# Kernel tuning notes

Measured on AMD Instinct MI355X. Metric: run time of the kernel, lower is better.

Reference implementation:

```python
import jax, jax.numpy as jnp
import numpy as np

NUM_LAYERS = 4
HID = 512
EMB = 512
VOCAB = 50000
SOU_LEN = 256
TAR_LEN = 50
BATCH = 8
VEXT = VOCAB + SOU_LEN


def _gru_layer(x, h0, wih, whh, bih, bhh):
    # x: [B,T,in], h0: [B,H]; PyTorch GRU gate order: r, z, n
    def step(h, xt):
        gi = xt @ wih.T + bih
        gh = h @ whh.T + bhh
        ir, iz, inn = jnp.split(gi, 3, axis=-1)
        hr, hz, hn = jnp.split(gh, 3, axis=-1)
        r = jax.nn.sigmoid(ir + hr)
        z = jax.nn.sigmoid(iz + hz)
        n = jnp.tanh(inn + r * hn)
        h_new = (1.0 - z) * n + z * h
        return h_new, h_new
    _, ys = jax.lax.scan(step, h0, jnp.swapaxes(x, 0, 1))
    return jnp.swapaxes(ys, 0, 1)


def _forward(sou, tar, hidden, encoder_outputs, extended_length,
             emb, gru_wih, gru_whh, gru_bih, gru_bhh,
             fc_enc_w, fc_enc_b, fc_dec_w, fc_dec_b, v_w,
             fc_out1_w, fc_out1_b, fc_out2_w, fc_out2_b,
             g1_w, g1_b, g2_w, g2_b, g3_w, g3_b):
    emb = emb.at[0].set(0.0)  # padding_idx=0 (also zeroes its grad)
    tar_emb = emb[tar]  # [B,T,E]
    # pack_padded_sequence: only first `length` steps processed, rest padded with 0
    lengths = jnp.maximum(jnp.sum(tar > 0, axis=-1), 1)
    x = tar_emb
    for l in range(gru_wih.shape[0]):
        x = _gru_layer(x, hidden[l], gru_wih[l], gru_whh[l], gru_bih[l], gru_bhh[l])
    t_idx = jnp.arange(x.shape[1])
    dec_out = jnp.where((t_idx[None, :] < lengths[:, None])[:, :, None], x, 0.0)  # [B,T,H]
    # additive (Bahdanau) attention
    e1 = encoder_outputs @ fc_enc_w.T + fc_enc_b          # [B,S,H]
    e2 = dec_out @ fc_dec_w.T + fc_dec_b                  # [B,T,H]
    energy = jnp.tanh(e1[:, None, :, :] + e2[:, :, None, :])  # [B,T,S,H]
    scores = jnp.einsum('btsh,h->bts', energy, v_w)
    scores = jnp.where((sou == 0)[:, None, :], -jnp.inf, scores)
    atten = jax.nn.softmax(scores, axis=-1)               # [B,T,S]
    weighted = jnp.einsum('bts,bsh->bth', atten, encoder_outputs)
    all_out = jnp.concatenate([weighted, dec_out], axis=-1)  # [B,T,2H]
    mid = all_out @ fc_out2_w.T + fc_out2_b
    logits = mid @ fc_out1_w.T + fc_out1_b                # [B,T,VEXT]
    # extended-vocab mask (vectorized version of the per-batch python loop)
    col = jnp.arange(logits.shape[-1])
    valid = col[None, None, :] < (VOCAB + extended_length)[:, None, None]
    logits = jnp.where(valid, logits, -1e9)
    output_gen = jax.nn.softmax(logits, axis=-1)
    # copy mechanism: scatter-add attention into extended vocab (replaces sparse one-hot bmm)
    def _scatter(att_b, sou_b):
        return jnp.zeros((att_b.shape[0], VEXT), att_b.dtype).at[:, sou_b].add(att_b)
    output_copy = jax.vmap(_scatter)(atten, sou)          # [B,T,VEXT]
    gate = jax.nn.sigmoid(
        jnp.einsum('bth,h->bt', weighted, g1_w) + g1_b[0]
        + jnp.einsum('bth,h->bt', dec_out, g2_w) + g2_b[0]
        + jnp.einsum('bte,e->bt', tar_emb, g3_w) + g3_b[0])[:, :, None]
    output = (1.0 - gate) * output_gen + gate * output_copy
    return output, atten


def setup_inputs() -> dict:
    key = jax.random.key(0)
    ks = jax.random.split(key, 24)
    s = 0.02
    return {
        'sou': jax.random.randint(ks[0], (BATCH, SOU_LEN), 0, VEXT),
        'tar': jax.random.randint(ks[1], (BATCH, TAR_LEN), 0, VEXT),
        'hidden': jax.random.normal(ks[2], (NUM_LAYERS, BATCH, HID), jnp.float32),
        'encoder_outputs': jax.random.normal(ks[3], (BATCH, SOU_LEN, HID), jnp.float32),
        'extended_length': jax.random.randint(ks[4], (BATCH,), 0, SOU_LEN),
        'emb': jax.random.normal(ks[5], (VEXT, EMB), jnp.float32) * s,
        'gru_wih': jax.random.normal(ks[6], (NUM_LAYERS, 3 * HID, EMB), jnp.float32) * s,
        'gru_whh': jax.random.normal(ks[7], (NUM_LAYERS, 3 * HID, HID), jnp.float32) * s,
        'gru_bih': jax.random.normal(ks[8], (NUM_LAYERS, 3 * HID), jnp.float32) * s,
        'gru_bhh': jax.random.normal(ks[9], (NUM_LAYERS, 3 * HID), jnp.float32) * s,
        'fc_enc_w': jax.random.normal(ks[10], (HID, HID), jnp.float32) * s,
        'fc_enc_b': jax.random.normal(ks[11], (HID,), jnp.float32) * s,
        'fc_dec_w': jax.random.normal(ks[12], (HID, HID), jnp.float32) * s,
        'fc_dec_b': jax.random.normal(ks[13], (HID,), jnp.float32) * s,
        'v_w': jax.random.normal(ks[14], (HID,), jnp.float32) * s,
        'fc_out1_w': jax.random.normal(ks[15], (VEXT, HID), jnp.float32) * s,
        'fc_out1_b': jax.random.normal(ks[16], (VEXT,), jnp.float32) * s,
        'fc_out2_w': jax.random.normal(ks[17], (HID, 2 * HID), jnp.float32) * s,
        'fc_out2_b': jax.random.normal(ks[18], (HID,), jnp.float32) * s,
        'g1_w': jax.random.normal(ks[19], (HID,), jnp.float32) * s,
        'g1_b': jnp.zeros((1,), jnp.float32),
        'g2_w': jax.random.normal(ks[20], (HID,), jnp.float32) * s,
        'g2_b': jnp.zeros((1,), jnp.float32),
        'g3_w': jax.random.normal(ks[21], (EMB,), jnp.float32) * s,
        'g3_b': jnp.zeros((1,), jnp.float32),
    }


def reference(sou, tar, hidden, encoder_outputs, extended_length,
              emb, gru_wih, gru_whh, gru_bih, gru_bhh,
              fc_enc_w, fc_enc_b, fc_dec_w, fc_dec_b, v_w,
              fc_out1_w, fc_out1_b, fc_out2_w, fc_out2_b,
              g1_w, g1_b, g2_w, g2_b, g3_w, g3_b):
    return _forward(sou, tar, hidden, encoder_outputs, extended_length,
                    emb, gru_wih, gru_whh, gru_bih, gru_bhh,
                    fc_enc_w, fc_enc_b, fc_dec_w, fc_dec_b, v_w,
                    fc_out1_w, fc_out1_b, fc_out2_w, fc_out2_b,
                    g1_w, g1_b, g2_w, g2_b, g3_w, g3_b)
```

## Files before the change

kernel.cpp:

```cpp
#include <hip/hip_runtime.h>

typedef unsigned short u16;
typedef unsigned int u32;

using bf16x8 = __attribute__((ext_vector_type(8))) short;
using f32x4  = __attribute__((ext_vector_type(4))) float;

#define VOCAB 50000
#define VEXT  50256
#define OUT_AT_OFF 20102400L

__device__ __forceinline__ u16 f2b(float f) {
  u32 x = __float_as_uint(f);
  u32 r = (x + 0x7fffu + ((x >> 16) & 1u)) >> 16;
  return (u16)r;
}

__global__ void k_conv(const float* __restrict__ src, u16* __restrict__ dst,
                       long realN, long totalN) {
  long i = (long)blockIdx.x * 256 + threadIdx.x;
  if (i >= totalN) return;
  float v = (i < realN) ? src[i] : 0.f;
  dst[i] = f2b(v);
}

__global__ void k_h0b(const float* __restrict__ hidden, u16* __restrict__ h0B) {
  int i = blockIdx.x * 256 + threadIdx.x;
  int l = i >> 13, rem = i & 8191, rr = rem >> 9, k = rem & 511;
  float v = (rr < 8) ? hidden[((long)l * 8 + rr) * 512 + k] : 0.f;
  h0B[i] = f2b(v);
}

__global__ __launch_bounds__(256) void k_prep(const int* __restrict__ tar,
                                              const float* __restrict__ emb,
                                              const float* __restrict__ g3w,
                                              u16* __restrict__ xB0,
                                              float* __restrict__ g3dot) {
  int r = blockIdx.x;
  int tid = threadIdx.x;
  int idx = tar[r];
  __shared__ float red[256];
  float p = 0.f;
  for (int k = tid; k < 512; k += 256) {
    float v = (idx == 0) ? 0.f : emb[(long)idx * 512 + k];
    xB0[(long)r * 512 + k] = f2b(v);
    p += v * g3w[k];
  }
  red[tid] = p; __syncthreads();
  for (int o = 128; o > 0; o >>= 1) { if (tid < o) red[tid] += red[tid + o]; __syncthreads(); }
  if (tid == 0) g3dot[r] = red[0];
}

__global__ void k_lengths(const int* __restrict__ tar, int* __restrict__ lens) {
  int b = threadIdx.x;
  if (b < 8) {
    int c = 0;
    for (int t = 0; t < 50; t++) c += (tar[b * 50 + t] > 0) ? 1 : 0;
    lens[b] = (c > 0) ? c : 1;
  }
}

__global__ __launch_bounds__(256) void k_mask(float* __restrict__ x4f,
                                              const int* __restrict__ lens) {
  int r = blockIdx.x, b = r / 50, t = r % 50;
  if (t >= lens[b])
    for (int k = threadIdx.x; k < 512; k += 256) x4f[(long)r * 512 + k] = 0.f;
}

__device__ __forceinline__ void wait_flags(const int* f, int target) {
  const int lane = threadIdx.x & 63;
  const int* p = f + (lane & 31) * 16;
  unsigned it = 0;
  while (true) {
    int v = __hip_atomic_load(p, __ATOMIC_RELAXED, __HIP_MEMORY_SCOPE_AGENT);
    if (__all(v >= target)) break;
    __builtin_amdgcn_s_sleep(4);
    if (++it > (1u << 20)) break;
  }
  __builtin_amdgcn_fence(__ATOMIC_ACQUIRE, "agent");
}

__global__ __launch_bounds__(128, 1) void k_gru(
    const u16* __restrict__ wihB, const u16* __restrict__ whhB,
    const float* __restrict__ bih, const float* __restrict__ bhh,
    const float* __restrict__ hidden, const u16* __restrict__ h0B,
    u16* __restrict__ xB,
    u16* __restrict__ hB,
    float* __restrict__ x4f,
    int* __restrict__ flags)
{
  const int wg = blockIdx.x;
  const int l = wg >> 5;
  const int wg32 = wg & 31;
  const int c0 = wg32 << 4;
  const int tid = threadIdx.x;
  const int wv = tid >> 6;
  const int lane = tid & 63;
  const int lrow = lane & 15;
  const int q = lane >> 4;

  __shared__ float giX[2][3][16][16];

  const u16* Wsrc = (wv == 0 ? wihB : whhB) + (long)l * 1536 * 512;
  bf16x8 bw[3][16];
#pragma unroll
  for (int g = 0; g < 3; g++)
#pragma unroll
    for (int ks = 0; ks < 16; ks++)
      bw[g][ks] = *(const bf16x8*)(Wsrc + (long)(g * 512 + c0 + lrow) * 512 + ks * 32 + q * 8);
#pragma unroll
  for (int g = 0; g < 3; g++)
#pragma unroll
    for (int ks = 0; ks < 16; ks++)
      asm volatile("" : "+v"(bw[g][ks]));

  const int col = c0 + lrow;
  const float bir = bih[l * 1536 + col],         bhr = bhh[l * 1536 + col];
  const float biz = bih[l * 1536 + 512 + col],   bhz = bhh[l * 1536 + 512 + col];
  const float bin_ = bih[l * 1536 + 1024 + col], bhn = bhh[l * 1536 + 1024 + col];

  const u16* xin = xB + (long)l * 16 * 50 * 512;

  float hreg[4];
  if (wv == 1) {
#pragma unroll
    for (int rg = 0; rg < 4; rg++) {
      int bb = q * 4 + rg;
      hreg[rg] = (bb < 8) ? hidden[((long)l * 8 + bb) * 512 + col] : 0.f;
    }
  }

  for (int t = 0; t < 50; t++) {
    const u16* Asrc;
    if (wv == 0) {
      if (l > 0) wait_flags(flags + (l - 1) * 512, t + 1);
      Asrc = xin + (long)lrow * 50 * 512 + (long)t * 512;
    } else {
      if (t > 0) wait_flags(flags + l * 512, t);
      Asrc = (t == 0) ? (h0B + ((long)l * 16 + lrow) * 512)
                      : (hB + (((long)l * 2 + ((t - 1) & 1)) * 16 + lrow) * 512);
    }

    bf16x8 af[16];
#pragma unroll
    for (int ks = 0; ks < 16; ks++) af[ks] = *(const bf16x8*)(Asrc + ks * 32 + q * 8);

    f32x4 a0 = {0.f, 0.f, 0.f, 0.f}, a1 = {0.f, 0.f, 0.f, 0.f}, a2 = {0.f, 0.f, 0.f, 0.f};
#pragma unroll
    for (int ks = 0; ks < 16; ks++) {
      a0 = __builtin_amdgcn_mfma_f32_16x16x32_bf16(af[ks], bw[0][ks], a0, 0, 0, 0);
      a1 = __builtin_amdgcn_mfma_f32_16x16x32_bf16(af[ks], bw[1][ks], a1, 0, 0, 0);
      a2 = __builtin_amdgcn_mfma_f32_16x16x32_bf16(af[ks], bw[2][ks], a2, 0, 0, 0);
    }

    if (wv == 0) {
#pragma unroll
      for (int rg = 0; rg < 4; rg++) {
        giX[t & 1][0][q * 4 + rg][lrow] = a0[rg];
        giX[t & 1][1][q * 4 + rg][lrow] = a1[rg];
        giX[t & 1][2][q * 4 + rg][lrow] = a2[rg];
      }
    }
    __syncthreads();

    if (wv == 1) {
#pragma unroll
      for (int rg = 0; rg < 4; rg++) {
        int bb = q * 4 + rg;
        if (bb < 8) {
          float gir = giX[t & 1][0][bb][lrow] + bir;
          float giz = giX[t & 1][1][bb][lrow] + biz;
          float gin = giX[t & 1][2][bb][lrow] + bin_;
          float ghr = a0[rg] + bhr;
          float ghz = a1[rg] + bhz;
          float ghn = a2[rg] + bhn;
          float hprev = hreg[rg];
          float rr = 1.f / (1.f + expf(-(gir + ghr)));
          float zz = 1.f / (1.f + expf(-(giz + ghz)));
          float nn = tanhf(gin + rr * ghn);
          float hnew = (1.f - zz) * nn + zz * hprev;
          hreg[rg] = hnew;
          long slot = ((long)l * 2 + (t & 1)) * 16 + bb;
          u16 hb16 = f2b(hnew);
          hB[slot * 512 + col] = hb16;
          if (l < 3) xB[(((long)(l + 1) * 16 + bb) * 50 + t) * 512 + col] = hb16;
          else       x4f[((long)bb * 50 + t) * 512 + col] = hnew;
        }
      }
      if (lane == 0)
        __hip_atomic_store(flags + ((long)l * 32 + wg32) * 16, t + 1,
                           __ATOMIC_RELEASE, __HIP_MEMORY_SCOPE_AGENT);
    }
  }
}

__global__ __launch_bounds__(256, 2) void k_gemm_bf16(
    const u16* __restrict__ A, const u16* __restrict__ Bm,
    const float* __restrict__ bias, float* __restrict__ C,
    int M, int N, int K, int ldc)
{
  __shared__ __align__(16) u16 As[4096];
  __shared__ __align__(16) u16 Bs[4096];
  const int tid = threadIdx.x;
  const int wv = tid >> 6, lane = tid & 63;
  const int wm = wv >> 1, wn = wv & 1;
  const int lrow = lane & 15, q = lane >> 4;
  const int m0 = blockIdx.y * 128, n0 = blockIdx.x * 128;

  f32x4 acc[4][4];
#pragma unroll
  for (int i = 0; i < 4; i++)
#pragma unroll
    for (int j = 0; j < 4; j++) acc[i][j] = {0.f, 0.f, 0.f, 0.f};

  for (int k0 = 0; k0 < K; k0 += 32) {
#pragma unroll
    for (int i = 0; i < 2; i++) {
      int c = i * 256 + tid;
      int row = c >> 2, ko = (c & 3) << 3;
      *(uint4*)(As + c * 8) = *(const uint4*)(A + (long)(m0 + row) * K + k0 + ko);
      *(uint4*)(Bs + c * 8) = *(const uint4*)(Bm + (long)(n0 + row) * K + k0 + ko);
    }
    __syncthreads();
    bf16x8 af[4], bfr[4];
#pragma unroll
    for (int i = 0; i < 4; i++) af[i] = *(const bf16x8*)(As + (wm * 64 + i * 16 + lrow) * 32 + q * 8);
#pragma unroll
    for (int j = 0; j < 4; j++) bfr[j] = *(const bf16x8*)(Bs + (wn * 64 + j * 16 + lrow) * 32 + q * 8);
#pragma unroll
    for (int i = 0; i < 4; i++)
#pragma unroll
      for (int j = 0; j < 4; j++)
        acc[i][j] = __builtin_amdgcn_mfma_f32_16x16x32_bf16(af[i], bfr[j], acc[i][j], 0, 0, 0);
    __syncthreads();
  }

#pragma unroll
  for (int i = 0; i < 4; i++) {
    int rbase = m0 + wm * 64 + i * 16 + q * 4;
#pragma unroll
    for (int j = 0; j < 4; j++) {
      int colg = n0 + wn * 64 + j * 16 + lrow;
      if (colg < N) {
        float bv = bias[colg];
#pragma unroll
        for (int rg = 0; rg < 4; rg++) {
          int rowg = rbase + rg;
          if (rowg < M) C[(long)rowg * ldc + colg] = acc[i][j][rg] + bv;
        }
      }
    }
  }
}

__global__ __launch_bounds__(256) void k_attn(
    const float* __restrict__ e1, const float* __restrict__ e2,
    const float* __restrict__ enc, const float* __restrict__ x4f,
    const int* __restrict__ sou, const float* __restrict__ vw,
    const float* __restrict__ g1w, const float* __restrict__ g1b,
    const float* __restrict__ g2w, const float* __restrict__ g2b,
    const float* __restrict__ g3b, const float* __restrict__ g3dot,
    float* __restrict__ all_out, float* __restrict__ gate,
    float* __restrict__ atten_out)
{
  int r = blockIdx.x;
  int b = r / 50;
  int tid = threadIdx.x;
  __shared__ float e2s[512], decs[512], at[256], red[256];
  for (int k = tid; k < 512; k += 256) {
    e2s[k] = e2[(long)r * 512 + k];
    decs[k] = x4f[(long)r * 512 + k];
  }
  __syncthreads();
  const float* erow = e1 + ((long)b * 256 + tid) * 512;
  float sc = 0.f;
#pragma unroll 4
  for (int h = 0; h < 512; h++) sc += vw[h] * tanhf(erow[h] + e2s[h]);
  if (sou[b * 256 + tid] == 0) sc = -INFINITY;

  red[tid] = sc; __syncthreads();
  for (int o = 128; o > 0; o >>= 1) { if (tid < o) red[tid] = fmaxf(red[tid], red[tid + o]); __syncthreads(); }
  float mx = red[0]; __syncthreads();
  float p = expf(sc - mx);
  red[tid] = p; __syncthreads();
  for (int o = 128; o > 0; o >>= 1) { if (tid < o) red[tid] += red[tid + o]; __syncthreads(); }
  float S = red[0]; __syncthreads();
  float a = p / S;
  at[tid] = a;
  atten_out[(long)r * 256 + tid] = a;
  __syncthreads();

  float pg = 0.f;
  for (int h = tid; h < 512; h += 256) {
    float wsum = 0.f;
    const float* ecol = enc + (long)b * 256 * 512 + h;
    for (int s = 0; s < 256; s++) wsum += at[s] * ecol[(long)s * 512];
    all_out[(long)r * 1024 + h] = wsum;
    all_out[(long)r * 1024 + 512 + h] = decs[h];
    pg += wsum * g1w[h] + decs[h] * g2w[h];
  }
  red[tid] = pg; __syncthreads();
  for (int o = 128; o > 0; o >>= 1) { if (tid < o) red[tid] += red[tid + o]; __syncthreads(); }
  if (tid == 0) {
    float z = red[0] + g1b[0] + g2b[0] + g3dot[r] + g3b[0];
    gate[r] = 1.f / (1.f + expf(-z));
  }
}

__global__ __launch_bounds__(1024) void k_softmax(float* __restrict__ out,
                                                  const float* __restrict__ gate,
                                                  const int* __restrict__ ext) {
  int r = blockIdx.x;
  int b = r / 50;
  int tid = threadIdx.x;
  int nv = VOCAB + ext[b];
  __shared__ float red[1024];
  float* row = out + (long)r * VEXT;
  float m = -INFINITY;
  for (int c = tid; c < nv; c += 1024) m = fmaxf(m, row[c]);
  red[tid] = m; __syncthreads();
  for (int o = 512; o > 0; o >>= 1) { if (tid < o) red[tid] = fmaxf(red[tid], red[tid + o]); __syncthreads(); }
  m = red[0]; __syncthreads();
  float s = 0.f;
  for (int c = tid; c < nv; c += 1024) s += expf(row[c] - m);
  red[tid] = s; __syncthreads();
  for (int o = 512; o > 0; o >>= 1) { if (tid < o) red[tid] += red[tid + o]; __syncthreads(); }
  float inv = (1.f - gate[r]) / red[0];
  for (int c = tid; c < VEXT; c += 1024) {
    float v = (c < nv) ? expf(row[c] - m) * inv : 0.f;
    row[c] = v;
  }
}

__global__ void k_scatter(float* __restrict__ out, const float* __restrict__ atten,
                          const float* __restrict__ gate, const int* __restrict__ sou) {
  int r = blockIdx.x, s = threadIdx.x;
  int b = r / 50;
  float v = gate[r] * atten[(long)r * 256 + s];
  int colv = sou[b * 256 + s];
  atomicAdd(out + (long)r * VEXT + colv, v);
}

extern "C" void kernel_launch(void* const* d_in, const int* in_sizes, int n_in,
                              void* d_out, int out_size, void* d_ws, size_t ws_size,
                              hipStream_t stream) {
  (void)in_sizes; (void)n_in; (void)out_size;
  const int* sou = (const int*)d_in[0];
  const int* tar = (const int*)d_in[1];
  const float* hidden = (const float*)d_in[2];
  const float* enc = (const float*)d_in[3];
  const int* ext = (const int*)d_in[4];
  const float* emb = (const float*)d_in[5];
  const float* wih = (const float*)d_in[6];
  const float* whh = (const float*)d_in[7];
  const float* bih = (const float*)d_in[8];
  const float* bhh = (const float*)d_in[9];
  const float* fc_enc_w = (const float*)d_in[10];
  const float* fc_enc_b = (const float*)d_in[11];
  const float* fc_dec_w = (const float*)d_in[12];
  const float* fc_dec_b = (const float*)d_in[13];
  const float* v_w = (const float*)d_in[14];
  const float* w1 = (const float*)d_in[15];
  const float* b1 = (const float*)d_in[16];
  const float* w2 = (const float*)d_in[17];
  const float* b2 = (const float*)d_in[18];
  const float* g1w = (const float*)d_in[19];
  const float* g1b = (const float*)d_in[20];
  const float* g2w = (const float*)d_in[21];
  const float* g2b = (const float*)d_in[22];
  const float* g3w = (const float*)d_in[23];
  const float* g3b = (const float*)d_in[24];
  float* out = (float*)d_out;

  char* base = (char*)d_ws;
  size_t cur = 0;
  auto alloc = [&](size_t bytes) -> void* {
    void* r = base + cur;
    cur = (cur + bytes + 255) & ~(size_t)255;
    return r;
  };
  u16* wihB = (u16*)alloc(6291456);
  u16* whhB = (u16*)alloc(6291456);
  u16* w1B  = (u16*)alloc(51511296);
  u16* encB = (u16*)alloc(2097152);
  u16* fceB = (u16*)alloc(524288);
  u16* fcdB = (u16*)alloc(524288);
  u16* fo2B = (u16*)alloc(1048576);
  u16* midB = (u16*)alloc(524288);
  u16* decB = (u16*)alloc(524288);
  u16* allB = (u16*)alloc(1048576);
  u16* xB   = (u16*)alloc(3276800);
  u16* h0B  = (u16*)alloc(65536);
  u16* hB   = (u16*)alloc(131072);
  float* x4f = (float*)alloc(819200);
  float* e1 = (float*)alloc(4194304);
  float* e2 = (float*)alloc(819200);
  float* allo = (float*)alloc(1638400);
  float* mid = (float*)alloc(819200);
  float* g3dot = (float*)alloc(1600);
  float* gate = (float*)alloc(1600);
  int* lens = (int*)alloc(32);
  int* flags = (int*)alloc(8192);
  if (cur > ws_size) return;

  hipMemsetAsync(flags, 0, 8192, stream);

  k_conv<<<12288, 256, 0, stream>>>(wih, wihB, 3145728L, 3145728L);
  k_conv<<<12288, 256, 0, stream>>>(whh, whhB, 3145728L, 3145728L);
  k_conv<<<100608, 256, 0, stream>>>(w1, w1B, 25731072L, 25755648L);
  k_conv<<<4096, 256, 0, stream>>>(enc, encB, 1048576L, 1048576L);
  k_conv<<<1024, 256, 0, stream>>>(fc_enc_w, fceB, 262144L, 262144L);
  k_conv<<<1024, 256, 0, stream>>>(fc_dec_w, fcdB, 262144L, 262144L);
  k_conv<<<2048, 256, 0, stream>>>(w2, fo2B, 524288L, 524288L);
  k_h0b<<<128, 256, 0, stream>>>(hidden, h0B);
  k_prep<<<400, 256, 0, stream>>>(tar, emb, g3w, xB, g3dot);
  k_lengths<<<1, 64, 0, stream>>>(tar, lens);

  k_gru<<<128, 128, 0, stream>>>(wihB, whhB, bih, bhh, hidden, h0B, xB, hB, x4f, flags);
  k_mask<<<400, 256, 0, stream>>>(x4f, lens);
  k_conv<<<1024, 256, 0, stream>>>(x4f, decB, 204800L, 262144L);

  k_gemm_bf16<<<dim3(4, 16), 256, 0, stream>>>(encB, fceB, fc_enc_b, e1, 2048, 512, 512, 512);
  k_gemm_bf16<<<dim3(4, 4), 256, 0, stream>>>(decB, fcdB, fc_dec_b, e2, 400, 512, 512, 512);
  k_attn<<<400, 256, 0, stream>>>(e1, e2, enc, x4f, sou, v_w, g1w, g1b, g2w, g2b, g3b,
                                  g3dot, allo, gate, out + OUT_AT_OFF);
  k_conv<<<2048, 256, 0, stream>>>(allo, allB, 409600L, 524288L);
  k_gemm_bf16<<<dim3(4, 4), 256, 0, stream>>>(allB, fo2B, b2, mid, 400, 512, 1024, 512);
  k_conv<<<1024, 256, 0, stream>>>(mid, midB, 204800L, 262144L);

  k_gemm_bf16<<<dim3(393, 4), 256, 0, stream>>>(midB, w1B, b1, out, 400, 50256, 512, 50256);
  k_softmax<<<400, 1024, 0, stream>>>(out, gate, ext);
  k_scatter<<<400, 256, 0, stream>>>(out, out + OUT_AT_OFF, gate, sou);
}
```

Before: 1.183 ms.

## Use system-scope atomic loads/stores for GRU hidden exchange and drop register-resident weights

The persistent GRU kernel now exchanges hidden states and layer outputs through relaxed system-scope atomic 32-bit loads and stores of packed bf16 pairs. This replaces plain stores plus an agent-scope acquire fence, which avoids cache invalidation on each wait. The weight fragments are no longer held in registers across timesteps and are instead reloaded from global memory inside the MFMA loop every step. The spin-wait sleep is also shortened. The changes aim to cut cross-workgroup synchronisation latency, but they add repeated weight traffic per step and depend on system-scope coherence for correctness.

Result: slower. 1.224 ms (+3.5%).

```diff
diff --git a/kernel.cpp b/kernel.cpp
--- a/kernel.cpp
+++ b/kernel.cpp
@@ -14,6 +14,19 @@
   u32 x = __float_as_uint(f);
   u32 r = (x + 0x7fffu + ((x >> 16) & 1u)) >> 16;
   return (u16)r;
+}
+
+__device__ __forceinline__ u32 sload(const u32* p) {
+  return __hip_atomic_load(p, __ATOMIC_RELAXED, __HIP_MEMORY_SCOPE_SYSTEM);
+}
+__device__ __forceinline__ void sstore(u32* p, u32 v) {
+  __hip_atomic_store(p, v, __ATOMIC_RELAXED, __HIP_MEMORY_SCOPE_SYSTEM);
+}
+__device__ __forceinline__ bf16x8 sload8(const u32* p) {
+  union { u32 u[4]; bf16x8 v; } x;
+  x.u[0] = sload(p); x.u[1] = sload(p + 1);
+  x.u[2] = sload(p + 2); x.u[3] = sload(p + 3);
+  return x.v;
 }
 
 __global__ void k_conv(const float* __restrict__ src, u16* __restrict__ dst,
@@ -67,17 +80,17 @@
     for (int k = threadIdx.x; k < 512; k += 256) x4f[(long)r * 512 + k] = 0.f;
 }
 
-__device__ __forceinline__ void wait_flags(const int* f, int target) {
+__device__ __forceinline__ void wait_flags(const u32* f, u32 target) {
   const int lane = threadIdx.x & 63;
-  const int* p = f + (lane & 31) * 16;
+  const u32* p = f + (lane & 31) * 16;
   unsigned it = 0;
   while (true) {
-    int v = __hip_atomic_load(p, __ATOMIC_RELAXED, __HIP_MEMORY_SCOPE_AGENT);
-    if (__all(v >= target)) break;
-    __builtin_amdgcn_s_sleep(4);
+    u32 v = sload(p);
+    if (__all((int)(v >= target))) break;
+    __builtin_amdgcn_s_sleep(2);
     if (++it > (1u << 20)) break;
   }
-  __builtin_amdgcn_fence(__ATOMIC_ACQUIRE, "agent");
+  asm volatile("" ::: "memory");
 }
 
 __global__ __launch_bounds__(128, 1) void k_gru(
@@ -85,9 +98,9 @@
     const float* __restrict__ bih, const float* __restrict__ bhh,
     const float* __restrict__ hidden, const u16* __restrict__ h0B,
     u16* __restrict__ xB,
-    u16* __restrict__ hB,
+    u32* __restrict__ hX,
     float* __restrict__ x4f,
-    int* __restrict__ flags)
+    u32* __restrict__ flags)
 {
   const int wg = blockIdx.x;
   const int l = wg >> 5;
@@ -102,17 +115,6 @@
   __shared__ float giX[2][3][16][16];
 
   const u16* Wsrc = (wv == 0 ? wihB : whhB) + (long)l * 1536 * 512;
-  bf16x8 bw[3][16];
-#pragma unroll
-  for (int g = 0; g < 3; g++)
-#pragma unroll
-    for (int ks = 0; ks < 16; ks++)
-      bw[g][ks] = *(const bf16x8*)(Wsrc + (long)(g * 512 + c0 + lrow) * 512 + ks * 32 + q * 8);
-#pragma unroll
-  for (int g = 0; g < 3; g++)
-#pragma unroll
-    for (int ks = 0; ks < 16; ks++)
-      asm volatile("" : "+v"(bw[g][ks]));
 
   const int col = c0 + lrow;
   const float bir = bih[l * 1536 + col],         bhr = bhh[l * 1536 + col];
@@ -120,6 +122,8 @@
   const float bin_ = bih[l * 1536 + 1024 + col], bhn = bhh[l * 1536 + 1024 + col];
 
   const u16* xin = xB + (long)l * 16 * 50 * 512;
+  u32* xBu = (u32*)xB;
+  u32* x4u = (u32*)x4f;
 
   float hreg[4];
   if (wv == 1) {
@@ -131,26 +135,40 @@
   }
 
   for (int t = 0; t < 50; t++) {
-    const u16* Asrc;
+    bf16x8 af[16];
     if (wv == 0) {
-      if (l > 0) wait_flags(flags + (l - 1) * 512, t + 1);
-      Asrc = xin + (long)lrow * 50 * 512 + (long)t * 512;
+      if (l > 0) {
+        wait_flags(flags + (l - 1) * 512, (u32)(t + 1));
+        const u32* As32 = (const u32*)xin + (long)lrow * 50 * 256 + (long)t * 256;
+#pragma unroll
+        for (int ks = 0; ks < 16; ks++) af[ks] = sload8(As32 + ks * 16 + q * 4);
+      } else {
+        const u16* Asrc = xin + (long)lrow * 50 * 512 + (long)t * 512;
+#pragma unroll
+        for (int ks = 0; ks < 16; ks++) af[ks] = *(const bf16x8*)(Asrc + ks * 32 + q * 8);
+      }
     } else {
-      if (t > 0) wait_flags(flags + l * 512, t);
-      Asrc = (t == 0) ? (h0B + ((long)l * 16 + lrow) * 512)
-                      : (hB + (((long)l * 2 + ((t - 1) & 1)) * 16 + lrow) * 512);
-    }
-
-    bf16x8 af[16];
-#pragma unroll
-    for (int ks = 0; ks < 16; ks++) af[ks] = *(const bf16x8*)(Asrc + ks * 32 + q * 8);
+      if (t > 0) {
+        wait_flags(flags + l * 512, (u32)t);
+        const u32* Hs = hX + (((long)l * 2 + ((t - 1) & 1)) * 16 + lrow) * 256;
+#pragma unroll
+        for (int ks = 0; ks < 16; ks++) af[ks] = sload8(Hs + ks * 16 + q * 4);
+      } else {
+        const u16* Asrc = h0B + ((long)l * 16 + lrow) * 512;
+#pragma unroll
+        for (int ks = 0; ks < 16; ks++) af[ks] = *(const bf16x8*)(Asrc + ks * 32 + q * 8);
+      }
+    }
 
     f32x4 a0 = {0.f, 0.f, 0.f, 0.f}, a1 = {0.f, 0.f, 0.f, 0.f}, a2 = {0.f, 0.f, 0.f, 0.f};
 #pragma unroll
     for (int ks = 0; ks < 16; ks++) {
-      a0 = __builtin_amdgcn_mfma_f32_16x16x32_bf16(af[ks], bw[0][ks], a0, 0, 0, 0);
-      a1 = __builtin_amdgcn_mfma_f32_16x16x32_bf16(af[ks], bw[1][ks], a1, 0, 0, 0);
-      a2 = __builtin_amdgcn_mfma_f32_16x16x32_bf16(af[ks], bw[2][ks], a2, 0, 0, 0);
+      bf16x8 b0 = *(const bf16x8*)(Wsrc + (long)(0 * 512 + c0 + lrow) * 512 + ks * 32 + q * 8);
+      bf16x8 b1 = *(const bf16x8*)(Wsrc + (long)(1 * 512 + c0 + lrow) * 512 + ks * 32 + q * 8);
+      bf16x8 b2 = *(const bf16x8*)(Wsrc + (long)(2 * 512 + c0 + lrow) * 512 + ks * 32 + q * 8);
+      a0 = __builtin_amdgcn_mfma_f32_16x16x32_bf16(af[ks], b0, a0, 0, 0, 0);
+      a1 = __builtin_amdgcn_mfma_f32_16x16x32_bf16(af[ks], b1, a1, 0, 0, 0);
+      a2 = __builtin_amdgcn_mfma_f32_16x16x32_bf16(af[ks], b2, a2, 0, 0, 0);
     }
 
     if (wv == 0) {
@@ -167,6 +185,8 @@
 #pragma unroll
       for (int rg = 0; rg < 4; rg++) {
         int bb = q * 4 + rg;
+        float hnew = 0.f;
+        u16 hb16 = 0;
         if (bb < 8) {
           float gir = giX[t & 1][0][bb][lrow] + bir;
           float giz = giX[t & 1][1][bb][lrow] + biz;
@@ -178,18 +198,26 @@
           float rr = 1.f / (1.f + expf(-(gir + ghr)));
           float zz = 1.f / (1.f + expf(-(giz + ghz)));
           float nn = tanhf(gin + rr * ghn);
-          float hnew = (1.f - zz) * nn + zz * hprev;
+          hnew = (1.f - zz) * nn + zz * hprev;
           hreg[rg] = hnew;
-          long slot = ((long)l * 2 + (t & 1)) * 16 + bb;
-          u16 hb16 = f2b(hnew);
-          hB[slot * 512 + col] = hb16;
-          if (l < 3) xB[(((long)(l + 1) * 16 + bb) * 50 + t) * 512 + col] = hb16;
-          else       x4f[((long)bb * 50 + t) * 512 + col] = hnew;
+          hb16 = f2b(hnew);
+        }
+        int other = __shfl_xor((int)hb16, 1);
+        if (bb < 8) {
+          if ((lane & 1) == 0) {
+            u32 pr = (u32)hb16 | ((u32)(u16)other << 16);
+            long slot = ((long)l * 2 + (t & 1)) * 16 + bb;
+            sstore(hX + slot * 256 + (col >> 1), pr);
+            if (l < 3)
+              sstore(xBu + (((long)(l + 1) * 16 + bb) * 50 + t) * 256 + (col >> 1), pr);
+          }
+          if (l == 3)
+            sstore(x4u + ((long)bb * 50 + t) * 512 + col, __float_as_uint(hnew));
         }
       }
       if (lane == 0)
-        __hip_atomic_store(flags + ((long)l * 32 + wg32) * 16, t + 1,
-                           __ATOMIC_RELEASE, __HIP_MEMORY_SCOPE_AGENT);
+        __hip_atomic_store(flags + ((long)l * 32 + wg32) * 16, (u32)(t + 1),
+                           __ATOMIC_RELEASE, __HIP_MEMORY_SCOPE_SYSTEM);
     }
   }
 }
@@ -391,7 +419,7 @@
   u16* allB = (u16*)alloc(1048576);
   u16* xB   = (u16*)alloc(3276800);
   u16* h0B  = (u16*)alloc(65536);
-  u16* hB   = (u16*)alloc(131072);
+  u32* hX   = (u32*)alloc(131072);
   float* x4f = (float*)alloc(819200);
   float* e1 = (float*)alloc(4194304);
   float* e2 = (float*)alloc(819200);
@@ -400,7 +428,7 @@
   float* g3dot = (float*)alloc(1600);
   float* gate = (float*)alloc(1600);
   int* lens = (int*)alloc(32);
-  int* flags = (int*)alloc(8192);
+  u32* flags = (u32*)alloc(8192);
   if (cur > ws_size) return;
 
   hipMemsetAsync(flags, 0, 8192, stream);
@@ -416,7 +444,7 @@
   k_prep<<<400, 256, 0, stream>>>(tar, emb, g3w, xB, g3dot);
   k_lengths<<<1, 64, 0, stream>>>(tar, lens);
 
-  k_gru<<<128, 128, 0, stream>>>(wihB, whhB, bih, bhh, hidden, h0B, xB, hB, x4f, flags);
+  k_gru<<<128, 128, 0, stream>>>(wihB, whhB, bih, bhh, hidden, h0B, xB, hX, x4f, flags);
   k_mask<<<400, 256, 0, stream>>>(x4f, lens);
   k_conv<<<1024, 256, 0, stream>>>(x4f, decB, 204800L, 262144L);
 
```
